# Optimization experiments

Hardware: AMD Instinct MI355X
Metric: run time of the kernel (lower is better)

The kernel has to match this reference:

```python
import jax, jax.numpy as jnp
import numpy as np

H = 64  # LSTM hidden size per direction


def _lstm_dir(x, Wih, Whh, b, reverse):
    # x: [B,T,I]; Wih: [4H,I]; Whh: [4H,H]; b: [4H] (b_ih + b_hh combined)
    if reverse:
        x = x[:, ::-1]
    xg = jnp.einsum('bti,gi->btg', x, Wih) + b  # precompute input gates [B,T,4H]
    B = x.shape[0]
    WhhT = Whh.T  # [H,4H]

    def step(carry, xt_g):
        h, c = carry
        g = xt_g + h @ WhhT  # [B,4H]
        i, f, gg, o = jnp.split(g, 4, axis=-1)  # PyTorch gate order i,f,g,o
        c = jax.nn.sigmoid(f) * c + jax.nn.sigmoid(i) * jnp.tanh(gg)
        h = jax.nn.sigmoid(o) * jnp.tanh(c)
        return (h, c), h

    h0 = jnp.zeros((B, H), x.dtype)
    _, hs = jax.lax.scan(step, (h0, h0), jnp.swapaxes(xg, 0, 1))
    hs = jnp.swapaxes(hs, 0, 1)  # [B,T,H]
    if reverse:
        hs = hs[:, ::-1]
    return hs


def _bilstm(x, wih_f, whh_f, b_f, wih_b, whh_b, b_b):
    fwd = _lstm_dir(x, wih_f, whh_f, b_f, False)
    bwd = _lstm_dir(x, wih_b, whh_b, b_b, True)
    return jnp.concatenate([fwd, bwd], axis=-1)  # [B,T,2H]


def setup_inputs() -> dict:
    key = jax.random.key(0)
    ks = jax.random.split(key, 16)
    B, IN = 8192, 20

    def w(k, shape, fan_in):
        return jax.random.normal(k, shape, jnp.float32) * (1.0 / np.sqrt(fan_in))

    inp = {
        'x': jax.random.normal(ks[0], (B, IN), jnp.float32),
        'fc1_w': w(ks[1], (50, IN), IN),
        'fc1_b': jnp.zeros((50,), jnp.float32),
        # rnn1: input_size=1, bidirectional
        'r1_wih_f': w(ks[2], (4 * H, 1), 1),
        'r1_whh_f': w(ks[3], (4 * H, H), H),
        'r1_b_f': jnp.zeros((4 * H,), jnp.float32),
        'r1_wih_b': w(ks[4], (4 * H, 1), 1),
        'r1_whh_b': w(ks[5], (4 * H, H), H),
        'r1_b_b': jnp.zeros((4 * H,), jnp.float32),
        # rnn2: input_size=2H=128, bidirectional
        'r2_wih_f': w(ks[6], (4 * H, 2 * H), 2 * H),
        'r2_whh_f': w(ks[7], (4 * H, H), H),
        'r2_b_f': jnp.zeros((4 * H,), jnp.float32),
        'r2_wih_b': w(ks[8], (4 * H, 2 * H), 2 * H),
        'r2_whh_b': w(ks[9], (4 * H, H), H),
        'r2_b_b': jnp.zeros((4 * H,), jnp.float32),
        'fc2_w': w(ks[10], (1, 2 * H), 2 * H),
        'fc2_b': jnp.zeros((1,), jnp.float32),
    }
    return inp


def reference(x, fc1_w, fc1_b,
              r1_wih_f, r1_whh_f, r1_b_f, r1_wih_b, r1_whh_b, r1_b_b,
              r2_wih_f, r2_whh_f, r2_b_f, r2_wih_b, r2_whh_b, r2_b_b,
              fc2_w, fc2_b):
    h = x @ fc1_w.T + fc1_b            # [B,50]
    h = h[..., None]                   # [B,50,1]
    h = _bilstm(h, r1_wih_f, r1_whh_f, r1_b_f, r1_wih_b, r1_whh_b, r1_b_b)  # [B,50,128]
    h = jnp.repeat(h, 2, axis=1)       # nearest upsample x2 along time -> [B,100,128]
    h = _bilstm(h, r2_wih_f, r2_whh_f, r2_b_f, r2_wih_b, r2_whh_b, r2_b_b)  # [B,100,128]
    out = jnp.tanh(jnp.einsum('btf,of->bto', h, fc2_w) + fc2_b)  # [B,100,1]
    return out
```

## Files before the change

kernel.cpp:

```cpp
#include <hip/hip_runtime.h>
#include <cmath>

#define H1    64
#define T1    50
#define T2    100
#define BATCH 8192
#define NB2   256
#define NTILE 512

typedef __attribute__((ext_vector_type(8))) short s16x8;
typedef __attribute__((ext_vector_type(4))) float f32x4;

#define MFMA16(a,b,c) __builtin_amdgcn_mfma_f32_16x16x32_bf16(a,b,c,0,0,0)

#define S_SIG  (-1.4426950408889634f)
#define S_TANH ( 2.8853900817779268f)

#define OFF_FC1T  ((size_t)0)
#define OFF_XF    ((size_t)1638400)
#define OFF_WA1   ((size_t)(1638400 + 104857600))
#define OFF_WA2HH (OFF_WA1 + 65536)
#define OFF_WA2IH (OFF_WA2HH + 65536)
#define OFF_PART  (OFF_WA2IH + 131072)
#define OFF_BS    (OFF_PART + 6553600)

__device__ __forceinline__ float rcp_(float x) { return __builtin_amdgcn_rcpf(x); }
__device__ __forceinline__ float exp2_(float x) {
#if __has_builtin(__builtin_amdgcn_exp2f)
    return __builtin_amdgcn_exp2f(x);
#else
    return exp2f(x);
#endif
}
__device__ __forceinline__ float sigp_(float e)  { return rcp_(1.f + exp2_(e)); }
__device__ __forceinline__ float tanhp_(float e) { return 1.f - 2.f * rcp_(1.f + exp2_(e)); }
__device__ __forceinline__ float tanhc_(float c) { return tanhp_(S_TANH * c); }
__device__ __forceinline__ float tanh_(float x)  { return tanhc_(x); }

__device__ __forceinline__ unsigned short bf16_rne(float x) {
    unsigned int u = __float_as_uint(x);
    u += 0x7fffu + ((u >> 16) & 1u);
    return (unsigned short)(u >> 16);
}

__device__ __forceinline__ unsigned int cvtpk_bf16(float a, float b) {
    unsigned int r;
    asm("v_cvt_pk_bf16_f32 %0, %1, %2" : "=v"(r) : "v"(a), "v"(b));
    return r;
}

__device__ __forceinline__ void bar_lgkm() {
    asm volatile("s_waitcnt lgkmcnt(0)\n\ts_barrier" ::: "memory");
}

#define CELL_PACK(ACC)                                                         \
        float hv[4];                                                           \
        _Pragma("unroll")                                                      \
        for (int r = 0; r < 4; ++r) {                                          \
            float Ei = exp2_(ACC[0][r]);                                       \
            float Ef = exp2_(ACC[1][r]);                                       \
            float Eg = exp2_(fminf(ACC[2][r], 100.f));                         \
            float Eo = exp2_(ACC[3][r]);                                       \
            float rf  = rcp_(1.f + Ef);                                        \
            float rig = rcp_((1.f + Ei) * (1.f + Eg));                         \
            float cc  = c4[r] * rf + (Eg - 1.f) * rig;                         \
            c4[r] = cc;                                                        \
            float Ec  = exp2_(fminf(S_TANH * cc, 100.f));                      \
            float roc = rcp_((1.f + Eo) * (1.f + Ec));                         \
            hv[r] = (Ec - 1.f) * roc;                                          \
        }                                                                      \
        uint2 vhi, vlo;                                                        \
        vhi.x = cvtpk_bf16(hv[0], hv[1]);                                      \
        vhi.y = cvtpk_bf16(hv[2], hv[3]);                                      \
        {                                                                      \
            float q0 = hv[0] - __uint_as_float(vhi.x << 16);                   \
            float q1 = hv[1] - __uint_as_float(vhi.x & 0xffff0000u);           \
            float q2 = hv[2] - __uint_as_float(vhi.y << 16);                   \
            float q3 = hv[3] - __uint_as_float(vhi.y & 0xffff0000u);           \
            vlo.x = cvtpk_bf16(q0, q1);                                        \
            vlo.y = cvtpk_bf16(q2, q3);                                        \
        }

__global__ __launch_bounds__(256) void k_pre(
    const float* __restrict__ whh1f, const float* __restrict__ whh1b,
    const float* __restrict__ whh2f, const float* __restrict__ whh2b,
    const float* __restrict__ wih2f, const float* __restrict__ wih2b,
    const float* __restrict__ b2f,   const float* __restrict__ b2b,
    const float* __restrict__ x, const float* __restrict__ fc1w,
    const float* __restrict__ fc1b,
    unsigned short* __restrict__ WA1, unsigned short* __restrict__ WA2HH,
    unsigned short* __restrict__ WA2IH, float* __restrict__ fc1T,
    float* __restrict__ part, float* __restrict__ BS)
{
    __shared__ float wls[1000];
    __shared__ float bls[50];
    int tid = threadIdx.x;
    int blk = blockIdx.x;
    if (blk < 64) {
        int i = blk * 256 + tid;
        if (i < 8192) {
            int a   = i >> 12;
            int r   = i & 4095;
            int dir = r >> 11, rem = r & 2047;
            int mt  = rem >> 7, rem2 = rem & 127;
            int kk  = rem2 >> 6, l = rem2 & 63;
            const float* s_ = a ? (dir ? whh2b : whh2f) : (dir ? whh1b : whh1f);
            unsigned short* d_ = a ? WA2HH : WA1;
            int gate = mt * 16 + (l & 15);
            float sc = ((gate >> 6) == 2) ? S_TANH : S_SIG;
            int k0   = kk * 32 + (l >> 4) * 8;
            const float* p = s_ + gate * 64 + k0;
            unsigned short* q = d_ + (size_t)r * 8;
#pragma unroll
            for (int j = 0; j < 8; ++j) q[j] = bf16_rne(p[j] * sc);
        } else {
            int r   = i - 8192;
            int dir = r >> 12, rem = r & 4095;
            int mt  = rem >> 8, rem2 = rem & 255;
            int kk  = rem2 >> 6, l = rem2 & 63;
            const float* s_ = dir ? wih2b : wih2f;
            int gate = mt * 16 + (l & 15);
            float sc = ((gate >> 6) == 2) ? S_TANH : S_SIG;
            int k0   = kk * 32 + (l >> 4) * 8;
            const float* p = s_ + gate * 128 + k0;
            unsigned short* q = WA2IH + (size_t)r * 8;
#pragma unroll
            for (int j = 0; j < 8; ++j) q[j] = bf16_rne(p[j] * sc);
        }
    } else if (blk < 96) {
        for (int i = tid; i < 1000; i += 256) wls[i] = fc1w[i];
        if (tid < 50) bls[tid] = fc1b[tid];
        __syncthreads();
        int bidx = (blk - 64) * 256 + tid;
        float xv[20];
#pragma unroll
        for (int i = 0; i < 20; ++i) xv[i] = x[bidx * 20 + i];
        for (int t = 0; t < T1; ++t) {
            float s = bls[t];
#pragma unroll
            for (int i = 0; i < 20; ++i) s += xv[i] * wls[t * 20 + i];
            fc1T[t * BATCH + bidx] = s;
        }
    } else if (blk < 352) {
        const int n = 2 * T2 * BATCH;
        for (int i = (blk - 96) * 256 + tid; i < n; i += 256 * 256) part[i] = 0.f;
    } else {
        for (int i = tid; i < 512; i += 256) {
            int d = i >> 8, m = i & 255;
            const float* bb = d ? b2b : b2f;
            float sc = ((m >> 6) == 2) ? S_TANH : S_SIG;
            BS[i] = bb[m] * sc;
        }
    }
}

__global__ __launch_bounds__(512, 4) void k_lstm1(
    const float* __restrict__ wih1f, const float* __restrict__ b1f,
    const float* __restrict__ wih1b, const float* __restrict__ b1b,
    const unsigned short* __restrict__ WA1,
    const float* __restrict__ fc1T,
    unsigned short* __restrict__ XF)
{
    __shared__ float x1s[T1][32];
    __shared__ unsigned short Htf[2][2][2][2][64][8];
    int tid  = threadIdx.x;
    int lane = tid & 63;
    int w    = __builtin_amdgcn_readfirstlane(tid >> 6);
    int wh   = w & 3, wsh = w >> 2;
    int quad = lane >> 4, col = lane & 15;
    int dir  = blockIdx.y, bblk = blockIdx.x;

    for (int i = tid; i < T1 * 32; i += 512) {
        int t = i >> 5, s = i & 31;
        x1s[t][s] = fc1T[t * BATCH + bblk * 32 + s];
    }
    {
        uint4* z = (uint4*)&Htf[0][0][0][0][0][0];
        uint4 zz; zz.x = 0u; zz.y = 0u; zz.z = 0u; zz.w = 0u;
        z[tid] = zz;
    }
    const float* wih = dir ? wih1b : wih1f;
    const float* bia = dir ? b1b : b1f;
    f32x4 wvv[4], bvv[4];
#pragma unroll
    for (int g = 0; g < 4; ++g) {
        float sc = (g == 2) ? S_TANH : S_SIG;
#pragma unroll
        for (int r = 0; r < 4; ++r) {
            int gate = g * 64 + wh * 16 + quad * 4 + r;
            wvv[g][r] = wih[gate] * sc;
            bvv[g][r] = bia[gate] * sc;
        }
    }
    s16x8 whhA[4][2];
#pragma unroll
    for (int g = 0; g < 4; ++g)
#pragma unroll
        for (int kk = 0; kk < 2; ++kk)
            whhA[g][kk] = *(const s16x8*)(WA1 +
                ((size_t)((dir * 16 + (g * 4 + wh)) * 2 + kk) * 64 + lane) * 8);

    float c4[4];
#pragma unroll
    for (int r = 0; r < 4; ++r) c4[r] = 0.f;

    int lq  = 2 * (wh & 1) + (quad >> 1);
    int lp  = lq * 16 + col;
    int jo  = (quad & 1) * 4;
    int kkw = wh >> 1;
    int kk1 = dir * 2 + kkw;
    int gtile = bblk * 2 + wsh;
    __syncthreads();

    int t = dir ? (T1 - 1) : 0;
    const int dt = dir ? -1 : 1;
    unsigned short* xfp = XF + ((((size_t)t * 4 + kk1) * NTILE + gtile) * 64 + lp) * 8 + jo;
    const ptrdiff_t xstep = (ptrdiff_t)dt * 4 * NTILE * 64 * 8;

#define L1_STEP(RB, WB)                                                        \
    {                                                                          \
        float xt = x1s[t][wsh * 16 + col];                                     \
        f32x4 acc[4];                                                          \
        _Pragma("unroll") for (int g = 0; g < 4; ++g)                          \
            _Pragma("unroll") for (int r = 0; r < 4; ++r)                      \
                acc[g][r] = bvv[g][r] + wvv[g][r] * xt;                        \
        {                                                                      \
            s16x8 hb00 = *(const s16x8*)&Htf[RB][0][0][wsh][lane][0];          \
            s16x8 hb01 = *(const s16x8*)&Htf[RB][0][1][wsh][lane][0];          \
            s16x8 hb10 = *(const s16x8*)&Htf[RB][1][0][wsh][lane][0];          \
            s16x8 hb11 = *(const s16x8*)&Htf[RB][1][1][wsh][lane][0];          \
            __builtin_amdgcn_s_setprio(1);                                     \
            _Pragma("unroll") for (int g = 0; g < 4; ++g) {                    \
                f32x4 a = MFMA16(whhA[g][0], hb00, acc[g]);                    \
                a = MFMA16(whhA[g][1], hb01, a);                               \
                a = MFMA16(whhA[g][0], hb10, a);                               \
                a = MFMA16(whhA[g][1], hb11, a);                               \
                acc[g] = a;                                                    \
            }                                                                  \
            __builtin_amdgcn_s_setprio(0);                                     \
        }                                                                      \
        CELL_PACK(acc)                                                         \
        *(uint2*)&Htf[WB][0][kkw][wsh][lp][jo] = vhi;                          \
        *(uint2*)&Htf[WB][1][kkw][wsh][lp][jo] = vlo;                          \
        *(uint2*)xfp = vhi;                                                    \
        xfp += xstep;                                                          \
        bar_lgkm();                                                            \
        t += dt;                                                               \
    }

    for (int it = 0; it < T1 / 2; ++it) {
        L1_STEP(0, 1)
        L1_STEP(1, 0)
    }
#undef L1_STEP
}

__global__ __launch_bounds__(512, 4) void k_lstm2(
    const float* __restrict__ BS,
    const float* __restrict__ fc2w,
    const unsigned short* __restrict__ WA2HH,
    const unsigned short* __restrict__ WA2IH,
    const unsigned short* __restrict__ XF,
    float* __restrict__ part)
{
    __shared__ unsigned short wAl[16][4][64][8];
    __shared__ unsigned short Htf[2][2][2][2][64][8];
    int tid  = threadIdx.x;
    int lane = tid & 63;
    int w    = __builtin_amdgcn_readfirstlane(tid >> 6);
    int wh   = w & 3, wsh = w >> 2;
    int quad = lane >> 4, col = lane & 15;
    int dir  = blockIdx.y, bblk = blockIdx.x;
    int gtile = bblk * 2 + wsh;

    {
        const uint4* src = (const uint4*)(WA2IH + (size_t)dir * 32768);
        uint4* dst = (uint4*)&wAl[0][0][0][0];
        for (int i = tid; i < 4096; i += 512) dst[i] = src[i];
    }
    {
        uint4* z = (uint4*)&Htf[0][0][0][0][0][0];
        uint4 zz; zz.x = 0u; zz.y = 0u; zz.z = 0u; zz.w = 0u;
        z[tid] = zz;
    }
    float f2v[4];
#pragma unroll
    for (int r = 0; r < 4; ++r)
        f2v[r] = fc2w[dir * 64 + wh * 16 + quad * 4 + r];

    s16x8 whhA[4][2];
#pragma unroll
    for (int g = 0; g < 4; ++g)
#pragma unroll
        for (int kk = 0; kk < 2; ++kk)
            whhA[g][kk] = *(const s16x8*)(WA2HH +
                ((size_t)((dir * 16 + (g * 4 + wh)) * 2 + kk) * 64 + lane) * 8);

    f32x4 bC[4];
    {
        const float* bsrc = BS + dir * 256 + wh * 16 + quad * 4;
#pragma unroll
        for (int g = 0; g < 4; ++g) {
            float4 b4 = *(const float4*)(bsrc + g * 64);
            bC[g][0] = b4.x; bC[g][1] = b4.y; bC[g][2] = b4.z; bC[g][3] = b4.w;
        }
    }

    float c4[4];
#pragma unroll
    for (int r = 0; r < 4; ++r) c4[r] = 0.f;

    int lq  = 2 * (wh & 1) + (quad >> 1);
    int lp  = lq * 16 + col;
    int jo  = (quad & 1) * 4;
    int kkw = wh >> 1;

    s16x8 xb[4];
    {
        int tp0 = dir ? (T1 - 1) : 0;
#pragma unroll
        for (int kk = 0; kk < 4; ++kk)
            xb[kk] = *(const s16x8*)(XF +
                (((size_t)(tp0 * 4 + kk) * NTILE + gtile) * 64 + lane) * 8);
    }
    f32x4 xacc[4];
    __syncthreads();

    int t2 = dir ? (T2 - 1) : 0;
    const int dt = dir ? -1 : 1;
    int tpn = dir ? (T1 - 2) : 1;

    float* pp = part + ((size_t)(dir * T2 + t2)) * BATCH + bblk * 32 + wsh * 16 + lane;
    const ptrdiff_t pstep = (ptrdiff_t)dt * BATCH;

#define L2_HIDCELL(RB, WB)                                                     \
    {                                                                          \
        s16x8 hb00 = *(const s16x8*)&Htf[RB][0][0][wsh][lane][0];              \
        s16x8 hb01 = *(const s16x8*)&Htf[RB][0][1][wsh][lane][0];              \
        s16x8 hb10 = *(const s16x8*)&Htf[RB][1][0][wsh][lane][0];              \
        s16x8 hb11 = *(const s16x8*)&Htf[RB][1][1][wsh][lane][0];              \
        f32x4 acc[4];                                                          \
        __builtin_amdgcn_s_setprio(1);                                         \
        _Pragma("unroll") for (int g = 0; g < 4; ++g) {                        \
            f32x4 a = MFMA16(whhA[g][0], hb00, xacc[g]);                       \
            a = MFMA16(whhA[g][1], hb01, a);                                   \
            a = MFMA16(whhA[g][0], hb10, a);                                   \
            a = MFMA16(whhA[g][1], hb11, a);                                   \
            acc[g] = a;                                                        \
        }                                                                      \
        __builtin_amdgcn_s_setprio(0);                                         \
        CELL_PACK(acc)                                                         \
        *(uint2*)&Htf[WB][0][kkw][wsh][lp][jo] = vhi;                          \
        *(uint2*)&Htf[WB][1][kkw][wsh][lp][jo] = vlo;                          \
        float pacc = f2v[0]*hv[0] + f2v[1]*hv[1] + f2v[2]*hv[2] + f2v[3]*hv[3];\
        pacc += __shfl_xor(pacc, 16);                                          \
        pacc += __shfl_xor(pacc, 32);                                          \
        if (lane < 16) atomicAdd(pp, pacc);                                    \
        pp += pstep;                                                           \
        bar_lgkm();                                                            \
        t2 += dt;                                                              \
    }

#define L2_EVEN()                                                              \
    {                                                                          \
        __builtin_amdgcn_s_setprio(1);                                         \
        _Pragma("unroll") for (int g = 0; g < 4; ++g) {                        \
            s16x8 wa0 = *(const s16x8*)&wAl[g * 4 + wh][0][lane][0];           \
            f32x4 a = MFMA16(wa0, xb[0], bC[g]);                               \
            _Pragma("unroll") for (int kk = 1; kk < 4; ++kk) {                 \
                s16x8 wa = *(const s16x8*)&wAl[g * 4 + wh][kk][lane][0];       \
                a = MFMA16(wa, xb[kk], a);                                     \
            }                                                                  \
            xacc[g] = a;                                                       \
        }                                                                      \
        __builtin_amdgcn_s_setprio(0);                                         \
    }

#define L2_PREF()                                                              \
    {                                                                          \
        _Pragma("unroll") for (int kk = 0; kk < 4; ++kk)                       \
            xb[kk] = *(const s16x8*)(XF +                                      \
                (((size_t)(tpn * 4 + kk) * NTILE + gtile) * 64 + lane) * 8);   \
        tpn += dt;                                                             \
        if (tpn < 0) tpn = 0;                                                  \
        if (tpn > T1 - 1) tpn = T1 - 1;                                        \
    }

    for (int it = 0; it < T2 / 4; ++it) {
        L2_EVEN()
        L2_HIDCELL(0, 1)
        L2_PREF()
        L2_HIDCELL(1, 0)
        L2_EVEN()
        L2_HIDCELL(0, 1)
        L2_PREF()
        L2_HIDCELL(1, 0)
    }
#undef L2_EVEN
#undef L2_PREF
#undef L2_HIDCELL
}

__global__ __launch_bounds__(256) void k_fc2(const float* __restrict__ part,
                                             const float* __restrict__ fc2b,
                                             float* __restrict__ out) {
    int u = blockIdx.x * 256 + threadIdx.x;
    if (u >= BATCH * T2) return;
    int b = u / T2, t = u - b * T2;
    float p = part[(size_t)t * BATCH + b] + part[((size_t)T2 + t) * BATCH + b] + fc2b[0];
    out[u] = tanh_(p);
}

extern "C" void kernel_launch(void* const* d_in, const int* in_sizes, int n_in,
                              void* d_out, int out_size, void* d_ws, size_t ws_size,
                              hipStream_t stream) {
    const float* x      = (const float*)d_in[0];
    const float* fc1w   = (const float*)d_in[1];
    const float* fc1b   = (const float*)d_in[2];
    const float* r1wihf = (const float*)d_in[3];
    const float* r1whhf = (const float*)d_in[4];
    const float* r1bf   = (const float*)d_in[5];
    const float* r1wihb = (const float*)d_in[6];
    const float* r1whhb = (const float*)d_in[7];
    const float* r1bb   = (const float*)d_in[8];
    const float* r2wihf = (const float*)d_in[9];
    const float* r2whhf = (const float*)d_in[10];
    const float* r2bf   = (const float*)d_in[11];
    const float* r2wihb = (const float*)d_in[12];
    const float* r2whhb = (const float*)d_in[13];
    const float* r2bb   = (const float*)d_in[14];
    const float* fc2w   = (const float*)d_in[15];
    const float* fc2b   = (const float*)d_in[16];
    char* ws   = (char*)d_ws;
    float* out = (float*)d_out;

    float*          fc1T  = (float*)(ws + OFF_FC1T);
    unsigned short* XF    = (unsigned short*)(ws + OFF_XF);
    unsigned short* WA1   = (unsigned short*)(ws + OFF_WA1);
    unsigned short* WA2HH = (unsigned short*)(ws + OFF_WA2HH);
    unsigned short* WA2IH = (unsigned short*)(ws + OFF_WA2IH);
    float*          partp = (float*)(ws + OFF_PART);
    float*          BS    = (float*)(ws + OFF_BS);

    k_pre<<<353, 256, 0, stream>>>(r1whhf, r1whhb, r2whhf, r2whhb, r2wihf, r2wihb,
                                   r2bf, r2bb, x, fc1w, fc1b,
                                   WA1, WA2HH, WA2IH, fc1T, partp, BS);
    dim3 g1(NB2, 2);
    k_lstm1<<<g1, 512, 0, stream>>>(r1wihf, r1bf, r1wihb, r1bb, WA1, fc1T, XF);
    k_lstm2<<<g1, 512, 0, stream>>>(BS, fc2w, WA2HH, WA2IH, XF, partp);
    k_fc2<<<(BATCH * T2 + 255) / 256, 256, 0, stream>>>(partp, fc2b, out);
}
```

Measured before the change: 354.0 us.

## Hold half of layer-2 input weights in registers and move bias to LDS

In the layer-2 LSTM kernel, the input-weight MFMA operands for gates 0-1 now live in registers, and only gates 2-3 are kept in LDS, which halves the weight LDS footprint and the LDS reads per even step. The bias moves from four f32x4 registers into a small shared array that is reloaded at each even step. The cell update also merges the forget and input reciprocals into a single rcp and clamps the exponents at 40, removing one transcendental per element. The trade-off is higher register pressure under launch_bounds(512,4), and the combined-denominator form changes the numerics slightly.

```diff
diff --git a/kernel.cpp b/kernel.cpp
--- a/kernel.cpp
+++ b/kernel.cpp
@@ -57,15 +57,16 @@
         float hv[4];                                                           \
         _Pragma("unroll")                                                      \
         for (int r = 0; r < 4; ++r) {                                          \
-            float Ei = exp2_(ACC[0][r]);                                       \
-            float Ef = exp2_(ACC[1][r]);                                       \
-            float Eg = exp2_(fminf(ACC[2][r], 100.f));                         \
+            float Ei = exp2_(fminf(ACC[0][r], 40.f));                          \
+            float Ef = exp2_(fminf(ACC[1][r], 40.f));                          \
+            float Eg = exp2_(fminf(ACC[2][r], 40.f));                          \
             float Eo = exp2_(ACC[3][r]);                                       \
-            float rf  = rcp_(1.f + Ef);                                        \
-            float rig = rcp_((1.f + Ei) * (1.f + Eg));                         \
-            float cc  = c4[r] * rf + (Eg - 1.f) * rig;                         \
+            float t12 = (1.f + Ei) * (1.f + Eg);                               \
+            float t3  = 1.f + Ef;                                              \
+            float rD  = rcp_(t12 * t3);                                        \
+            float cc  = (c4[r] * t12 + (Eg - 1.f) * t3) * rD;                  \
             c4[r] = cc;                                                        \
-            float Ec  = exp2_(fminf(S_TANH * cc, 100.f));                      \
+            float Ec  = exp2_(fminf(S_TANH * cc, 40.f));                       \
             float roc = rcp_((1.f + Eo) * (1.f + Ec));                         \
             hv[r] = (Ec - 1.f) * roc;                                          \
         }                                                                      \
@@ -263,8 +264,9 @@
     const unsigned short* __restrict__ XF,
     float* __restrict__ part)
 {
-    __shared__ unsigned short wAl[16][4][64][8];
+    __shared__ unsigned short wAl[8][4][64][8];
     __shared__ unsigned short Htf[2][2][2][2][64][8];
+    __shared__ __align__(16) float bsl[256];
     int tid  = threadIdx.x;
     int lane = tid & 63;
     int w    = __builtin_amdgcn_readfirstlane(tid >> 6);
@@ -274,10 +276,11 @@
     int gtile = bblk * 2 + wsh;
 
     {
-        const uint4* src = (const uint4*)(WA2IH + (size_t)dir * 32768);
+        const uint4* src = (const uint4*)(WA2IH + (size_t)dir * 32768 + 16384);
         uint4* dst = (uint4*)&wAl[0][0][0][0];
-        for (int i = tid; i < 4096; i += 512) dst[i] = src[i];
-    }
+        for (int i = tid; i < 2048; i += 512) dst[i] = src[i];
+    }
+    if (tid < 256) bsl[tid] = BS[dir * 256 + tid];
     {
         uint4* z = (uint4*)&Htf[0][0][0][0][0][0];
         uint4 zz; zz.x = 0u; zz.y = 0u; zz.z = 0u; zz.w = 0u;
@@ -296,15 +299,13 @@
             whhA[g][kk] = *(const s16x8*)(WA2HH +
                 ((size_t)((dir * 16 + (g * 4 + wh)) * 2 + kk) * 64 + lane) * 8);
 
-    f32x4 bC[4];
-    {
-        const float* bsrc = BS + dir * 256 + wh * 16 + quad * 4;
-#pragma unroll
-        for (int g = 0; g < 4; ++g) {
-            float4 b4 = *(const float4*)(bsrc + g * 64);
-            bC[g][0] = b4.x; bC[g][1] = b4.y; bC[g][2] = b4.z; bC[g][3] = b4.w;
-        }
-    }
+    s16x8 waR[2][4];
+#pragma unroll
+    for (int g = 0; g < 2; ++g)
+#pragma unroll
+        for (int kk = 0; kk < 4; ++kk)
+            waR[g][kk] = *(const s16x8*)(WA2IH +
+                ((size_t)(dir * 4096 + (g * 4 + wh) * 256 + kk * 64 + lane)) * 8);
 
     float c4[4];
 #pragma unroll
@@ -364,11 +365,18 @@
 #define L2_EVEN()                                                              \
     {                                                                          \
         __builtin_amdgcn_s_setprio(1);                                         \
-        _Pragma("unroll") for (int g = 0; g < 4; ++g) {                        \
-            s16x8 wa0 = *(const s16x8*)&wAl[g * 4 + wh][0][lane][0];           \
-            f32x4 a = MFMA16(wa0, xb[0], bC[g]);                               \
-            _Pragma("unroll") for (int kk = 1; kk < 4; ++kk) {                 \
-                s16x8 wa = *(const s16x8*)&wAl[g * 4 + wh][kk][lane][0];       \
+        _Pragma("unroll") for (int g = 0; g < 2; ++g) {                        \
+            f32x4 a = *(const f32x4*)&bsl[(g * 4 + wh) * 16 + quad * 4];       \
+            a = MFMA16(waR[g][0], xb[0], a);                                   \
+            a = MFMA16(waR[g][1], xb[1], a);                                   \
+            a = MFMA16(waR[g][2], xb[2], a);                                   \
+            a = MFMA16(waR[g][3], xb[3], a);                                   \
+            xacc[g] = a;                                                       \
+        }                                                                      \
+        _Pragma("unroll") for (int g = 2; g < 4; ++g) {                        \
+            f32x4 a = *(const f32x4*)&bsl[(g * 4 + wh) * 16 + quad * 4];       \
+            _Pragma("unroll") for (int kk = 0; kk < 4; ++kk) {                 \
+                s16x8 wa = *(const s16x8*)&wAl[(g - 2) * 4 + wh][kk][lane][0]; \
                 a = MFMA16(wa, xb[kk], a);                                     \
             }                                                                  \
             xacc[g] = a;                                                       \
```

Result: slower. 405.4 us (+14.5%).

## Split LSTM1 blocks to 16 batch rows with 256 threads and fuse cell reciprocals

Applied to the files above, without the earlier changes.

Layer-1 LSTM blocks now handle one 16-row batch tile with 4 waves instead of two tiles with 8 waves, and the grid doubles to 512x2 blocks. This drops the per-block wave-subgroup indexing and lets more, smaller blocks spread across CUs for the latency-bound recurrence. Layer 1 also gets a new cell variant that merges the forget and input/gate reciprocals into one rcp, with tighter exponent clamps to avoid overflow in the combined product. The extra multiplies and the clamp change slightly alter numerics, and smaller blocks mean more barrier-synchronised groups to schedule.

```diff
diff --git a/kernel.cpp b/kernel.cpp
--- a/kernel.cpp
+++ b/kernel.cpp
@@ -6,6 +6,7 @@
 #define T2    100
 #define BATCH 8192
 #define NB2   256
+#define NB1   512
 #define NTILE 512
 
 typedef __attribute__((ext_vector_type(8))) short s16x8;
@@ -53,7 +54,7 @@
     asm volatile("s_waitcnt lgkmcnt(0)\n\ts_barrier" ::: "memory");
 }
 
-#define CELL_PACK(ACC)                                                         \
+#define CELL_PACK_A(ACC)                                                       \
         float hv[4];                                                           \
         _Pragma("unroll")                                                      \
         for (int r = 0; r < 4; ++r) {                                          \
@@ -66,6 +67,35 @@
             float cc  = c4[r] * rf + (Eg - 1.f) * rig;                         \
             c4[r] = cc;                                                        \
             float Ec  = exp2_(fminf(S_TANH * cc, 100.f));                      \
+            float roc = rcp_((1.f + Eo) * (1.f + Ec));                         \
+            hv[r] = (Ec - 1.f) * roc;                                          \
+        }                                                                      \
+        uint2 vhi, vlo;                                                        \
+        vhi.x = cvtpk_bf16(hv[0], hv[1]);                                      \
+        vhi.y = cvtpk_bf16(hv[2], hv[3]);                                      \
+        {                                                                      \
+            float q0 = hv[0] - __uint_as_float(vhi.x << 16);                   \
+            float q1 = hv[1] - __uint_as_float(vhi.x & 0xffff0000u);           \
+            float q2 = hv[2] - __uint_as_float(vhi.y << 16);                   \
+            float q3 = hv[3] - __uint_as_float(vhi.y & 0xffff0000u);           \
+            vlo.x = cvtpk_bf16(q0, q1);                                        \
+            vlo.y = cvtpk_bf16(q2, q3);                                        \
+        }
+
+#define CELL_PACK_B(ACC)                                                       \
+        float hv[4];                                                           \
+        _Pragma("unroll")                                                      \
+        for (int r = 0; r < 4; ++r) {                                          \
+            float Ei = exp2_(fminf(ACC[0][r], 40.f));                          \
+            float Ef = exp2_(fminf(ACC[1][r], 40.f));                          \
+            float Eg = exp2_(fminf(ACC[2][r], 40.f));                          \
+            float Eo = exp2_(ACC[3][r]);                                       \
+            float t12 = (1.f + Ei) * (1.f + Eg);                               \
+            float t3  = 1.f + Ef;                                              \
+            float rD  = rcp_(t12 * t3);                                        \
+            float cc  = (c4[r] * t12 + (Eg - 1.f) * t3) * rD;                  \
+            c4[r] = cc;                                                        \
+            float Ec  = exp2_(fminf(S_TANH * cc, 40.f));                       \
             float roc = rcp_((1.f + Eo) * (1.f + Ec));                         \
             hv[r] = (Ec - 1.f) * roc;                                          \
         }                                                                      \
@@ -154,28 +184,27 @@
     }
 }
 
-__global__ __launch_bounds__(512, 4) void k_lstm1(
+__global__ __launch_bounds__(256, 4) void k_lstm1(
     const float* __restrict__ wih1f, const float* __restrict__ b1f,
     const float* __restrict__ wih1b, const float* __restrict__ b1b,
     const unsigned short* __restrict__ WA1,
     const float* __restrict__ fc1T,
     unsigned short* __restrict__ XF)
 {
-    __shared__ float x1s[T1][32];
-    __shared__ unsigned short Htf[2][2][2][2][64][8];
+    __shared__ float x1s[T1][16];
+    __shared__ unsigned short Htf[2][2][2][64][8];
     int tid  = threadIdx.x;
     int lane = tid & 63;
-    int w    = __builtin_amdgcn_readfirstlane(tid >> 6);
-    int wh   = w & 3, wsh = w >> 2;
+    int wh   = __builtin_amdgcn_readfirstlane(tid >> 6);
     int quad = lane >> 4, col = lane & 15;
     int dir  = blockIdx.y, bblk = blockIdx.x;
 
-    for (int i = tid; i < T1 * 32; i += 512) {
-        int t = i >> 5, s = i & 31;
-        x1s[t][s] = fc1T[t * BATCH + bblk * 32 + s];
+    for (int i = tid; i < T1 * 16; i += 256) {
+        int t = i >> 4, s = i & 15;
+        x1s[t][s] = fc1T[t * BATCH + bblk * 16 + s];
     }
     {
-        uint4* z = (uint4*)&Htf[0][0][0][0][0][0];
+        uint4* z = (uint4*)&Htf[0][0][0][0][0];
         uint4 zz; zz.x = 0u; zz.y = 0u; zz.z = 0u; zz.w = 0u;
         z[tid] = zz;
     }
@@ -209,7 +238,7 @@
     int jo  = (quad & 1) * 4;
     int kkw = wh >> 1;
     int kk1 = dir * 2 + kkw;
-    int gtile = bblk * 2 + wsh;
+    int gtile = bblk;
     __syncthreads();
 
     int t = dir ? (T1 - 1) : 0;
@@ -219,16 +248,16 @@
 
 #define L1_STEP(RB, WB)                                                        \
     {                                                                          \
-        float xt = x1s[t][wsh * 16 + col];                                     \
+        float xt = x1s[t][col];                                                \
         f32x4 acc[4];                                                          \
         _Pragma("unroll") for (int g = 0; g < 4; ++g)                          \
             _Pragma("unroll") for (int r = 0; r < 4; ++r)                      \
                 acc[g][r] = bvv[g][r] + wvv[g][r] * xt;                        \
         {                                                                      \
-            s16x8 hb00 = *(const s16x8*)&Htf[RB][0][0][wsh][lane][0];          \
-            s16x8 hb01 = *(const s16x8*)&Htf[RB][0][1][wsh][lane][0];          \
-            s16x8 hb10 = *(const s16x8*)&Htf[RB][1][0][wsh][lane][0];          \
-            s16x8 hb11 = *(const s16x8*)&Htf[RB][1][1][wsh][lane][0];          \
+            s16x8 hb00 = *(const s16x8*)&Htf[RB][0][0][lane][0];               \
+            s16x8 hb01 = *(const s16x8*)&Htf[RB][0][1][lane][0];               \
+            s16x8 hb10 = *(const s16x8*)&Htf[RB][1][0][lane][0];               \
+            s16x8 hb11 = *(const s16x8*)&Htf[RB][1][1][lane][0];               \
             __builtin_amdgcn_s_setprio(1);                                     \
             _Pragma("unroll") for (int g = 0; g < 4; ++g) {                    \
                 f32x4 a = MFMA16(whhA[g][0], hb00, acc[g]);                    \
@@ -239,9 +268,9 @@
             }                                                                  \
             __builtin_amdgcn_s_setprio(0);                                     \
         }                                                                      \
-        CELL_PACK(acc)                                                         \
-        *(uint2*)&Htf[WB][0][kkw][wsh][lp][jo] = vhi;                          \
-        *(uint2*)&Htf[WB][1][kkw][wsh][lp][jo] = vlo;                          \
+        CELL_PACK_B(acc)                                                       \
+        *(uint2*)&Htf[WB][0][kkw][lp][jo] = vhi;                               \
+        *(uint2*)&Htf[WB][1][kkw][lp][jo] = vlo;                               \
         *(uint2*)xfp = vhi;                                                    \
         xfp += xstep;                                                          \
         bar_lgkm();                                                            \
@@ -349,7 +378,7 @@
             acc[g] = a;                                                        \
         }                                                                      \
         __builtin_amdgcn_s_setprio(0);                                         \
-        CELL_PACK(acc)                                                         \
+        CELL_PACK_A(acc)                                                       \
         *(uint2*)&Htf[WB][0][kkw][wsh][lp][jo] = vhi;                          \
         *(uint2*)&Htf[WB][1][kkw][wsh][lp][jo] = vlo;                          \
         float pacc = f2v[0]*hv[0] + f2v[1]*hv[1] + f2v[2]*hv[2] + f2v[3]*hv[3];\
@@ -445,8 +474,9 @@
     k_pre<<<353, 256, 0, stream>>>(r1whhf, r1whhb, r2whhf, r2whhb, r2wihf, r2wihb,
                                    r2bf, r2bb, x, fc1w, fc1b,
                                    WA1, WA2HH, WA2IH, fc1T, partp, BS);
+    dim3 g1a(NB1, 2);
+    k_lstm1<<<g1a, 256, 0, stream>>>(r1wihf, r1bf, r1wihb, r1bb, WA1, fc1T, XF);
     dim3 g1(NB2, 2);
-    k_lstm1<<<g1, 512, 0, stream>>>(r1wihf, r1bf, r1wihb, r1bb, WA1, fc1T, XF);
     k_lstm2<<<g1, 512, 0, stream>>>(BS, fc2w, WA2HH, WA2IH, XF, partp);
     k_fc2<<<(BATCH * T2 + 255) / 256, 256, 0, stream>>>(partp, fc2b, out);
 }
```

New measurement: 358.5 us. Within noise of the previous version (+1.3%).

## Make layer-1 LSTM wave-local with cross-lane h exchange instead of LDS barriers

Applied to the files above, without the earlier changes.

Rewrites k_lstm1 so each wavefront owns a full 16-sample batch tile and computes all 16 gate tiles for it, keeping the whole Whh matrix in registers. The hidden state passes between steps through ds_bpermute shuffles inside the wave, which removes the shared-memory round trip and the per-step block barrier. The grid changes to 128x2 blocks of 256 threads at one block per SIMD set, and the cell math is reformulated with a single reciprocal for the f/i/g gates. The cost is much higher register pressure (32 A-fragments, 16 cell states), lower occupancy, and less latency hiding inside each serial chain.

```diff
diff --git a/kernel.cpp b/kernel.cpp
--- a/kernel.cpp
+++ b/kernel.cpp
@@ -6,6 +6,7 @@
 #define T2    100
 #define BATCH 8192
 #define NB2   256
+#define NB1   128
 #define NTILE 512
 
 typedef __attribute__((ext_vector_type(8))) short s16x8;
@@ -53,7 +54,7 @@
     asm volatile("s_waitcnt lgkmcnt(0)\n\ts_barrier" ::: "memory");
 }
 
-#define CELL_PACK(ACC)                                                         \
+#define CELL_PACK_A(ACC)                                                       \
         float hv[4];                                                           \
         _Pragma("unroll")                                                      \
         for (int r = 0; r < 4; ++r) {                                          \
@@ -154,105 +155,139 @@
     }
 }
 
-__global__ __launch_bounds__(512, 4) void k_lstm1(
+__global__ __launch_bounds__(256, 1) void k_lstm1(
     const float* __restrict__ wih1f, const float* __restrict__ b1f,
     const float* __restrict__ wih1b, const float* __restrict__ b1b,
     const unsigned short* __restrict__ WA1,
     const float* __restrict__ fc1T,
     unsigned short* __restrict__ XF)
 {
-    __shared__ float x1s[T1][32];
-    __shared__ unsigned short Htf[2][2][2][2][64][8];
+    __shared__ __align__(16) float WBw[16][16];
+    __shared__ __align__(16) float WBb[16][16];
+    __shared__ float x1s[4][T1][16];
     int tid  = threadIdx.x;
     int lane = tid & 63;
-    int w    = __builtin_amdgcn_readfirstlane(tid >> 6);
-    int wh   = w & 3, wsh = w >> 2;
-    int quad = lane >> 4, col = lane & 15;
+    int wv   = __builtin_amdgcn_readfirstlane(tid >> 6);
+    int col  = lane & 15, q = lane >> 4;
     int dir  = blockIdx.y, bblk = blockIdx.x;
-
-    for (int i = tid; i < T1 * 32; i += 512) {
-        int t = i >> 5, s = i & 31;
-        x1s[t][s] = fc1T[t * BATCH + bblk * 32 + s];
-    }
-    {
-        uint4* z = (uint4*)&Htf[0][0][0][0][0][0];
-        uint4 zz; zz.x = 0u; zz.y = 0u; zz.z = 0u; zz.w = 0u;
-        z[tid] = zz;
-    }
+    int gtile = bblk * 4 + wv;
+
     const float* wih = dir ? wih1b : wih1f;
     const float* bia = dir ? b1b : b1f;
-    f32x4 wvv[4], bvv[4];
-#pragma unroll
-    for (int g = 0; g < 4; ++g) {
+
+    if (tid < 256) {
+        int tile = tid >> 4, m = tid & 15;
+        int g = tile >> 2, hb = tile & 3;
+        int gate = g * 64 + hb * 16 + m;
         float sc = (g == 2) ? S_TANH : S_SIG;
-#pragma unroll
-        for (int r = 0; r < 4; ++r) {
-            int gate = g * 64 + wh * 16 + quad * 4 + r;
-            wvv[g][r] = wih[gate] * sc;
-            bvv[g][r] = bia[gate] * sc;
-        }
-    }
-    s16x8 whhA[4][2];
-#pragma unroll
-    for (int g = 0; g < 4; ++g)
+        WBw[tile][m] = wih[gate] * sc;
+        WBb[tile][m] = bia[gate] * sc;
+    }
+    for (int i = tid; i < T1 * 64; i += 256) {
+        int t = i >> 6, rem = i & 63;
+        x1s[rem >> 4][t][rem & 15] = fc1T[t * BATCH + bblk * 64 + rem];
+    }
+
+    s16x8 whA[16][2];
+#pragma unroll
+    for (int tile = 0; tile < 16; ++tile)
 #pragma unroll
         for (int kk = 0; kk < 2; ++kk)
-            whhA[g][kk] = *(const s16x8*)(WA1 +
-                ((size_t)((dir * 16 + (g * 4 + wh)) * 2 + kk) * 64 + lane) * 8);
-
-    float c4[4];
-#pragma unroll
-    for (int r = 0; r < 4; ++r) c4[r] = 0.f;
-
-    int lq  = 2 * (wh & 1) + (quad >> 1);
-    int lp  = lq * 16 + col;
-    int jo  = (quad & 1) * 4;
-    int kkw = wh >> 1;
-    int kk1 = dir * 2 + kkw;
-    int gtile = bblk * 2 + wsh;
-    __syncthreads();
+            whA[tile][kk] = *(const s16x8*)(WA1 +
+                ((size_t)((dir * 16 + tile) * 2 + kk) * 64 + lane) * 8);
+
+    float c4[4][4];
+#pragma unroll
+    for (int hb = 0; hb < 4; ++hb)
+#pragma unroll
+        for (int r = 0; r < 4; ++r) c4[hb][r] = 0.f;
+
+    s16x8 Bhi0 = {0,0,0,0,0,0,0,0}, Bhi1 = Bhi0, Blo0 = Bhi0, Blo1 = Bhi0;
+
+    int idxA = ((2 * (q & 1)) * 16 + col) * 4;
+    int idxB = idxA + 64;
+    bool qhi = (lane >= 32);
 
     int t = dir ? (T1 - 1) : 0;
     const int dt = dir ? -1 : 1;
-    unsigned short* xfp = XF + ((((size_t)t * 4 + kk1) * NTILE + gtile) * 64 + lp) * 8 + jo;
-    const ptrdiff_t xstep = (ptrdiff_t)dt * 4 * NTILE * 64 * 8;
-
-#define L1_STEP(RB, WB)                                                        \
-    {                                                                          \
-        float xt = x1s[t][wsh * 16 + col];                                     \
-        f32x4 acc[4];                                                          \
-        _Pragma("unroll") for (int g = 0; g < 4; ++g)                          \
-            _Pragma("unroll") for (int r = 0; r < 4; ++r)                      \
-                acc[g][r] = bvv[g][r] + wvv[g][r] * xt;                        \
-        {                                                                      \
-            s16x8 hb00 = *(const s16x8*)&Htf[RB][0][0][wsh][lane][0];          \
-            s16x8 hb01 = *(const s16x8*)&Htf[RB][0][1][wsh][lane][0];          \
-            s16x8 hb10 = *(const s16x8*)&Htf[RB][1][0][wsh][lane][0];          \
-            s16x8 hb11 = *(const s16x8*)&Htf[RB][1][1][wsh][lane][0];          \
-            __builtin_amdgcn_s_setprio(1);                                     \
-            _Pragma("unroll") for (int g = 0; g < 4; ++g) {                    \
-                f32x4 a = MFMA16(whhA[g][0], hb00, acc[g]);                    \
-                a = MFMA16(whhA[g][1], hb01, a);                               \
-                a = MFMA16(whhA[g][0], hb10, a);                               \
-                a = MFMA16(whhA[g][1], hb11, a);                               \
-                acc[g] = a;                                                    \
-            }                                                                  \
-            __builtin_amdgcn_s_setprio(0);                                     \
-        }                                                                      \
-        CELL_PACK(acc)                                                         \
-        *(uint2*)&Htf[WB][0][kkw][wsh][lp][jo] = vhi;                          \
-        *(uint2*)&Htf[WB][1][kkw][wsh][lp][jo] = vlo;                          \
-        *(uint2*)xfp = vhi;                                                    \
-        xfp += xstep;                                                          \
-        bar_lgkm();                                                            \
-        t += dt;                                                               \
-    }
-
-    for (int it = 0; it < T1 / 2; ++it) {
-        L1_STEP(0, 1)
-        L1_STEP(1, 0)
-    }
-#undef L1_STEP
+    unsigned short* xfp0 = XF +
+        ((((size_t)t * 4 + dir * 2 + 0) * NTILE + gtile) * 64 + lane) * 8;
+    unsigned short* xfp1 = xfp0 + (size_t)NTILE * 512;
+    const ptrdiff_t xstep = (ptrdiff_t)dt * 4 * NTILE * 512;
+
+    __syncthreads();
+
+    for (int step = 0; step < T1; ++step) {
+        float xt = x1s[wv][t][col];
+        unsigned phi[4][2], plo[4][2];
+#pragma unroll
+        for (int hb = 0; hb < 4; ++hb) {
+            f32x4 accs[4];
+#pragma unroll
+            for (int g = 0; g < 4; ++g) {
+                const int tile = g * 4 + hb;
+                f32x4 w4 = *(const f32x4*)&WBw[tile][4 * q];
+                f32x4 b4 = *(const f32x4*)&WBb[tile][4 * q];
+                f32x4 a;
+#pragma unroll
+                for (int r = 0; r < 4; ++r) a[r] = b4[r] + w4[r] * xt;
+                a = MFMA16(whA[tile][0], Bhi0, a);
+                a = MFMA16(whA[tile][1], Bhi1, a);
+                a = MFMA16(whA[tile][0], Blo0, a);
+                a = MFMA16(whA[tile][1], Blo1, a);
+                accs[g] = a;
+            }
+            {
+                float hv[4];
+#pragma unroll
+                for (int r = 0; r < 4; ++r) {
+                    float Ei = exp2_(fminf(accs[0][r], 40.f));
+                    float Ef = exp2_(fminf(accs[1][r], 40.f));
+                    float Eg = exp2_(fminf(accs[2][r], 40.f));
+                    float Eo = exp2_(accs[3][r]);
+                    float t12 = (1.f + Ei) * (1.f + Eg);
+                    float t3  = 1.f + Ef;
+                    float rD  = rcp_(t12 * t3);
+                    float cc  = (c4[hb][r] * t12 + (Eg - 1.f) * t3) * rD;
+                    c4[hb][r] = cc;
+                    float Ec  = exp2_(fminf(S_TANH * cc, 40.f));
+                    float roc = rcp_((1.f + Eo) * (1.f + Ec));
+                    hv[r] = (Ec - 1.f) * roc;
+                }
+                unsigned p0 = cvtpk_bf16(hv[0], hv[1]);
+                unsigned p1 = cvtpk_bf16(hv[2], hv[3]);
+                phi[hb][0] = p0; phi[hb][1] = p1;
+                float q0 = hv[0] - __uint_as_float(p0 << 16);
+                float q1 = hv[1] - __uint_as_float(p0 & 0xffff0000u);
+                float q2 = hv[2] - __uint_as_float(p1 << 16);
+                float q3 = hv[3] - __uint_as_float(p1 & 0xffff0000u);
+                plo[hb][0] = cvtpk_bf16(q0, q1);
+                plo[hb][1] = cvtpk_bf16(q2, q3);
+            }
+        }
+        union V { s16x8 v; unsigned u[4]; } nh0, nh1, nl0, nl1;
+#pragma unroll
+        for (int d = 0; d < 4; ++d) {
+            int idx = (d < 2) ? idxA : idxB;
+            int h0a = __builtin_amdgcn_ds_bpermute(idx, (int)phi[0][d & 1]);
+            int h0b = __builtin_amdgcn_ds_bpermute(idx, (int)phi[1][d & 1]);
+            nh0.u[d] = (unsigned)(qhi ? h0b : h0a);
+            int l0a = __builtin_amdgcn_ds_bpermute(idx, (int)plo[0][d & 1]);
+            int l0b = __builtin_amdgcn_ds_bpermute(idx, (int)plo[1][d & 1]);
+            nl0.u[d] = (unsigned)(qhi ? l0b : l0a);
+            int h1a = __builtin_amdgcn_ds_bpermute(idx, (int)phi[2][d & 1]);
+            int h1b = __builtin_amdgcn_ds_bpermute(idx, (int)phi[3][d & 1]);
+            nh1.u[d] = (unsigned)(qhi ? h1b : h1a);
+            int l1a = __builtin_amdgcn_ds_bpermute(idx, (int)plo[2][d & 1]);
+            int l1b = __builtin_amdgcn_ds_bpermute(idx, (int)plo[3][d & 1]);
+            nl1.u[d] = (unsigned)(qhi ? l1b : l1a);
+        }
+        Bhi0 = nh0.v; Bhi1 = nh1.v; Blo0 = nl0.v; Blo1 = nl1.v;
+        *(s16x8*)xfp0 = Bhi0;
+        *(s16x8*)xfp1 = Bhi1;
+        xfp0 += xstep; xfp1 += xstep;
+        t += dt;
+    }
 }
 
 __global__ __launch_bounds__(512, 4) void k_lstm2(
@@ -349,7 +384,7 @@
             acc[g] = a;                                                        \
         }                                                                      \
         __builtin_amdgcn_s_setprio(0);                                         \
-        CELL_PACK(acc)                                                         \
+        CELL_PACK_A(acc)                                                       \
         *(uint2*)&Htf[WB][0][kkw][wsh][lp][jo] = vhi;                          \
         *(uint2*)&Htf[WB][1][kkw][wsh][lp][jo] = vlo;                          \
         float pacc = f2v[0]*hv[0] + f2v[1]*hv[1] + f2v[2]*hv[2] + f2v[3]*hv[3];\
@@ -445,8 +480,9 @@
     k_pre<<<353, 256, 0, stream>>>(r1whhf, r1whhb, r2whhf, r2whhb, r2wihf, r2wihb,
                                    r2bf, r2bb, x, fc1w, fc1b,
                                    WA1, WA2HH, WA2IH, fc1T, partp, BS);
+    dim3 g1a(NB1, 2);
+    k_lstm1<<<g1a, 256, 0, stream>>>(r1wihf, r1bf, r1wihb, r1bb, WA1, fc1T, XF);
     dim3 g1(NB2, 2);
-    k_lstm1<<<g1, 512, 0, stream>>>(r1wihf, r1bf, r1wihb, r1bb, WA1, fc1T, XF);
     k_lstm2<<<g1, 512, 0, stream>>>(BS, fc2w, WA2HH, WA2IH, XF, partp);
     k_fc2<<<(BATCH * T2 + 255) / 256, 256, 0, stream>>>(partp, fc2b, out);
 }
```

After: 414.9 us. +17.2%, slower.
